# Kernel tuning notes

Measured on AMD Instinct MI355X. Metric: run time of the kernel, lower is better.

The kernel has to match this reference:

```python
import jax, jax.numpy as jnp
import numpy as np

B, C, H, W = 16, 384, 64, 64
S, R, GR = 16, 8, 64
EPS = 1e-6


def setup_inputs() -> dict:
    key = jax.random.key(0)
    ks = jax.random.split(key, 16)
    def rn(k, shape, s):
        return jax.random.normal(k, shape, dtype=jnp.float32) * s
    inp = {"x": jax.random.normal(ks[0], (B, C, H, W), dtype=jnp.float32)}
    i = 1
    for p in ("row", "col"):
        inp[p + "_a_logit"] = jnp.zeros((S,), jnp.float32)
        inp[p + "_U"] = rn(ks[i], (S, R), 0.02); i += 1
        inp[p + "_V"] = rn(ks[i], (S, R), 0.02); i += 1
        inp[p + "_Win"] = rn(ks[i], (S, C), 1.0 / np.sqrt(C)); i += 1
        inp[p + "_bin"] = jnp.zeros((S,), jnp.float32)
        inp[p + "_Wg"] = rn(ks[i], (S, C), 1.0 / np.sqrt(C)); i += 1
        inp[p + "_bg"] = jnp.zeros((S,), jnp.float32)
        inp[p + "_Wout"] = rn(ks[i], (C, S), 1.0 / np.sqrt(S)); i += 1
        inp[p + "_bout"] = jnp.zeros((C,), jnp.float32)
        inp[p + "_Wskip"] = rn(ks[i], (C, C), 1.0 / np.sqrt(C)); i += 1
        inp[p + "_bskip"] = jnp.zeros((C,), jnp.float32)
    inp["g1_w"] = rn(ks[i], (GR, C), 1.0 / np.sqrt(C)); i += 1
    inp["g1_b"] = jnp.zeros((GR,), jnp.float32)
    inp["g2_w"] = rn(ks[i], (C, GR), 1.0 / np.sqrt(GR)); i += 1
    inp["g2_b"] = jnp.zeros((C,), jnp.float32)
    inp["norm_w"] = jnp.ones((C,), jnp.float32)
    inp["norm_b"] = jnpp = jnp.zeros((C,), jnp.float32)
    inp["norm_b"] = jnp.zeros((C,), jnp.float32)
    return inp


def _ssm1d(x, a_logit, U, V, Win, bin_, Wg, bg, Wout, bout, Wskip, bskip, reverse):
    # x: [N, L, D]
    if reverse:
        x = x[:, ::-1]
    u = jnp.einsum('nld,sd->nls', x, Win) + bin_          # [N,L,S]
    g = jax.nn.sigmoid(jnp.einsum('nld,sd->nls', x, Wg) + bg)
    a = jax.nn.sigmoid(a_logit)                            # [S]
    # h_t = a*h + g_t*u_t + h @ (U V^T)^T  ==  h @ (diag(a) + (U V^T)^T) + g_t*u_t
    A = jnp.diag(a) + (U @ V.T).T                          # [S,S]
    gu = jnp.swapaxes(g * u, 0, 1)                         # [L,N,S]
    h0 = jnp.zeros((x.shape[0], a.shape[0]), x.dtype)

    def step(h, gu_t):
        h = h @ A + gu_t
        return h, h

    _, hs = jax.lax.scan(step, h0, gu)                     # [L,N,S]
    hs = jnp.swapaxes(hs, 0, 1)                            # [N,L,S]
    y = (jnp.einsum('nls,ds->nld', hs, Wout) + bout
         + jnp.einsum('nld,ed->nle', x, Wskip) + bskip)
    if reverse:
        y = y[:, ::-1]
    return y


def _forward(x, rp, cp, g1_w, g1_b, g2_w, g2_b, norm_w, norm_b):
    Bx, Cx, Hx, Wx = x.shape
    rows = jnp.transpose(x, (0, 2, 3, 1)).reshape(Bx * Hx, Wx, Cx)
    cols = jnp.transpose(x, (0, 3, 2, 1)).reshape(Bx * Wx, Hx, Cx)
    yr = _ssm1d(rows, *rp, False) + _ssm1d(rows, *rp, True)
    yc = _ssm1d(cols, *cp, False) + _ssm1d(cols, *cp, True)
    yr = jnp.transpose(yr.reshape(Bx, Hx, Wx, Cx), (0, 3, 1, 2))
    yc = jnp.transpose(yc.reshape(Bx, Wx, Hx, Cx), (0, 3, 2, 1))
    y = (yr + yc) * 0.25
    # LayerNorm over channel dim of BCHW
    mean = x.mean(axis=1, keepdims=True)
    var = ((x - mean) ** 2).mean(axis=1, keepdims=True)
    xn = (x - mean) / jnp.sqrt(var + EPS)
    xn = xn * norm_w[None, :, None, None] + norm_b[None, :, None, None]
    # gate: 1x1 conv -> GELU(exact) -> 1x1 conv -> sigmoid
    h1 = jax.nn.gelu(jnp.einsum('bchw,oc->bohw', xn, g1_w) + g1_b[None, :, None, None], approximate=False)
    g = jax.nn.sigmoid(jnp.einsum('bghw,cg->bchw', h1, g2_w) + g2_b[None, :, None, None])
    return g * y + (1.0 - g) * x


def reference(x, row_a_logit, row_U, row_V, row_Win, row_bin, row_Wg, row_bg, row_Wout, row_bout, row_Wskip, row_bskip, col_a_logit, col_U, col_V, col_Win, col_bin, col_Wg, col_bg, col_Wout, col_bout, col_Wskip, col_bskip, g1_w, g1_b, g2_w, g2_b, norm_w, norm_b):
    rp = (row_a_logit, row_U, row_V, row_Win, row_bin, row_Wg, row_bg, row_Wout, row_bout, row_Wskip, row_bskip)
    cp = (col_a_logit, col_U, col_V, col_Win, col_bin, col_Wg, col_bg, col_Wout, col_bout, col_Wskip, col_bskip)
    return _forward(x, rp, cp, g1_w, g1_b, g2_w, g2_b, norm_w, norm_b)
```

## Files before the change

### kernel.cpp

```cpp
#include <hip/hip_runtime.h>
#include <hip/hip_bf16.h>
#include <math.h>

#define PP 4096
#define CCH 384
#define NB 16

using short8 = __attribute__((ext_vector_type(8))) short;
using f32x4  = __attribute__((ext_vector_type(4))) float;
using half2t = __attribute__((ext_vector_type(2))) __fp16;

__device__ __forceinline__ float sigmoidf_(float v){ return 1.f/(1.f+expf(-v)); }
__device__ __forceinline__ float fast_sig(float v){
  return __builtin_amdgcn_rcpf(1.f + __builtin_amdgcn_exp2f(-v*1.44269504088896f));
}
__device__ __forceinline__ unsigned int f2bf(float f){
  __hip_bfloat16 h = __float2bfloat16(f);
  return (unsigned int)*reinterpret_cast<unsigned short*>(&h);
}
__device__ __forceinline__ float bf2f(unsigned short u){
  unsigned int w = ((unsigned int)u) << 16;
  return __uint_as_float(w);
}
__device__ __forceinline__ void gload_lds16(const void* g, void* l){
  __builtin_amdgcn_global_load_lds(
      (const __attribute__((address_space(1))) unsigned int*)g,
      (__attribute__((address_space(3))) unsigned int*)l, 16, 0, 0);
}

__global__ __launch_bounds__(256) void k_prep(
    const float* __restrict__ rAl, const float* __restrict__ rU, const float* __restrict__ rV,
    const float* __restrict__ cAl, const float* __restrict__ cU, const float* __restrict__ cV,
    const float* __restrict__ rWs, const float* __restrict__ cWs,
    const float* __restrict__ WinR, const float* __restrict__ WgR,
    const float* __restrict__ WinC, const float* __restrict__ WgC,
    const float* __restrict__ g1w, const float* __restrict__ nw, const float* __restrict__ nb,
    const float* __restrict__ g2w,
    const float* __restrict__ WoR, const float* __restrict__ WoC,
    float* __restrict__ Arow, float* __restrict__ Acol,
    unsigned short* __restrict__ WsumBf, unsigned short* __restrict__ WcatBf,
    unsigned short* __restrict__ g2wBf, unsigned short* __restrict__ WocatBf,
    float* __restrict__ t1, float* __restrict__ t2)
{
  int bid = blockIdx.x, tid = threadIdx.x;
  if (bid < 576) {
    int idx = bid*256 + tid;
    WsumBf[idx] = (unsigned short)f2bf(rWs[idx] + cWs[idx]);
  } else if (bid < 768) {
    int idx = (bid-576)*256 + tid;
    int row = idx / CCH, col = idx - row*CCH;
    float v;
    if      (row < 16)  v = WinR[row*CCH + col];
    else if (row < 32)  v = WgR [(row-16)*CCH + col];
    else if (row < 48)  v = WinC[(row-32)*CCH + col];
    else if (row < 64)  v = WgC [(row-48)*CCH + col];
    else                v = g1w[(row-64)*CCH + col]*nw[col];
    WcatBf[idx] = (unsigned short)f2bf(v);
  } else if (bid < 864) {
    int idx = (bid-768)*256 + tid;
    g2wBf[idx] = (unsigned short)f2bf(g2w[idx]);
  } else if (bid < 960) {
    int idx = (bid-864)*256 + tid;
    int c = idx >> 6, k = idx & 63;
    int sel = (k >> 4) & 1;
    float v = 0.5f * (sel ? WoC[c*16 + (k&15)] : WoR[c*16 + (k&15)]);
    WocatBf[idx] = (unsigned short)f2bf(v);
  } else {
    {
      int i = tid >> 4, j = tid & 15;
      float sr = 0.f, sc = 0.f;
      #pragma unroll
      for (int r=0;r<8;++r){ sr += rV[i*8+r]*rU[j*8+r]; sc += cV[i*8+r]*cU[j*8+r]; }
      if (i==j){ sr += sigmoidf_(rAl[i]); sc += sigmoidf_(cAl[i]); }
      Arow[tid] = sr; Acol[tid] = sc;
    }
    if (tid < 64) {
      float s1=0.f, s2=0.f;
      for (int c=0;c<CCH;++c){ s1 += g1w[tid*CCH+c]*nw[c]; s2 += nb[c]*g1w[tid*CCH+c]; }
      t1[tid]=s1; t2[tid]=s2;
    }
  }
}

__global__ __launch_bounds__(256) void k_xf(
    const float* __restrict__ x, const unsigned short* __restrict__ WcatBf,
    const float* __restrict__ binR, const float* __restrict__ bgR,
    const float* __restrict__ binC, const float* __restrict__ bgC,
    const float* __restrict__ t1, const float* __restrict__ t2,
    const float* __restrict__ g1b,
    unsigned short* __restrict__ xbf,
    float* __restrict__ ugr, float* __restrict__ ugc,
    unsigned short* __restrict__ h1bf)
{
  int b = blockIdx.x >> 6, pt = blockIdx.x & 63;
  int t = threadIdx.x;
  int w = t >> 6, l = t & 63;
  int lr = l & 15, kq = l >> 4, kb8 = kq*8;
  int pl = t & 63, g4 = w;

  __shared__ unsigned short xtb[2][64*64];
  __shared__ float red[512];
  __shared__ float meanS[64], invS[64];

  const float* xb = x + (size_t)b*CCH*PP + pt*64;
  f32x4 acc[2][4] = {};
  float sx = 0.f, sx2 = 0.f;

  const unsigned short* wrow0 = WcatBf + (size_t)(w*32 + lr)*CCH + kb8;
  const unsigned short* wrow1 = wrow0 + 16*CCH;
  unsigned short* xgo = xbf + ((size_t)(b*PP + pt*64))*CCH;

  float xv[16];
  #pragma unroll
  for (int j=0;j<16;++j) xv[j] = xb[(size_t)(g4*16 + j)*PP + pl];

  {
    unsigned int pk[8];
    #pragma unroll
    for (int j=0;j<16;++j){ sx += xv[j]; sx2 += xv[j]*xv[j]; }
    #pragma unroll
    for (int j=0;j<8;++j) pk[j] = f2bf(xv[2*j]) | (f2bf(xv[2*j+1])<<16);
    int kg0 = g4*2, kg1 = g4*2+1;
    *(uint4*)&xtb[0][(size_t)(pl*8 + (kg0 ^ (pl&7)))*8] = make_uint4(pk[0],pk[1],pk[2],pk[3]);
    *(uint4*)&xtb[0][(size_t)(pl*8 + (kg1 ^ (pl&7)))*8] = make_uint4(pk[4],pk[5],pk[6],pk[7]);
  }
  #pragma unroll
  for (int j=0;j<16;++j) xv[j] = xb[(size_t)(64 + g4*16 + j)*PP + pl];
  __syncthreads();

  #pragma unroll
  for (int cc=0; cc<6; ++cc) {
    int cur = cc & 1;
    if (cc < 5) {
      unsigned int pk[8];
      #pragma unroll
      for (int j=0;j<16;++j){ sx += xv[j]; sx2 += xv[j]*xv[j]; }
      #pragma unroll
      for (int j=0;j<8;++j) pk[j] = f2bf(xv[2*j]) | (f2bf(xv[2*j+1])<<16);
      int kg0 = g4*2, kg1 = g4*2+1;
      *(uint4*)&xtb[cur^1][(size_t)(pl*8 + (kg0 ^ (pl&7)))*8] = make_uint4(pk[0],pk[1],pk[2],pk[3]);
      *(uint4*)&xtb[cur^1][(size_t)(pl*8 + (kg1 ^ (pl&7)))*8] = make_uint4(pk[4],pk[5],pk[6],pk[7]);
      if (cc < 4) {
        #pragma unroll
        for (int j=0;j<16;++j) xv[j] = xb[(size_t)((cc+2)*64 + g4*16 + j)*PP + pl];
      }
    }
    short8 a0k0 = *(const short8*)(wrow0 + cc*64);
    short8 a0k1 = *(const short8*)(wrow0 + cc*64 + 32);
    short8 a1k0 = *(const short8*)(wrow1 + cc*64);
    short8 a1k1 = *(const short8*)(wrow1 + cc*64 + 32);
    #pragma unroll
    for (int ks=0; ks<2; ++ks){
      int kg = ks*4 + kq;
      #pragma unroll
      for (int nf=0; nf<4; ++nf){
        int pr = nf*16 + lr;
        short8 bv = *(const short8*)&xtb[cur][(size_t)(pr*8 + (kg ^ (pr&7)))*8];
        acc[0][nf] = __builtin_amdgcn_mfma_f32_16x16x32_bf16(ks? a0k1:a0k0, bv, acc[0][nf], 0,0,0);
        acc[1][nf] = __builtin_amdgcn_mfma_f32_16x16x32_bf16(ks? a1k1:a1k0, bv, acc[1][nf], 0,0,0);
      }
    }
    #pragma unroll
    for (int it=0; it<2; ++it){
      int p2 = 32*it + (t>>3), kg2 = t & 7;
      uint4 v = *(const uint4*)&xtb[cur][(size_t)(p2*8 + (kg2 ^ (p2&7)))*8];
      *(uint4*)&xgo[(size_t)p2*CCH + cc*64 + kg2*8] = v;
    }
    __syncthreads();
  }

  red[g4*64 + pl] = sx;
  red[256 + g4*64 + pl] = sx2;
  __syncthreads();
  if (t < 64) {
    float s1 = red[t] + red[64+t] + red[128+t] + red[192+t];
    float s2 = red[256+t] + red[320+t] + red[384+t] + red[448+t];
    float mu = s1 * (1.f/CCH);
    float var = s2 * (1.f/CCH) - mu*mu;
    meanS[t] = mu;
    invS[t]  = rsqrtf(var + 1e-6f);
  }
  __syncthreads();

  if (w < 2) {
    const float* bu = w ? binC : binR;
    const float* bg = w ? bgC  : bgR;
    float* dst = w ? ugc : ugr;
    float bus[4], bgs[4];
    #pragma unroll
    for (int r=0;r<4;++r){ int s = kq*4 + r; bus[r]=bu[s]; bgs[r]=bg[s]; }
    #pragma unroll
    for (int nf=0; nf<4; ++nf){
      size_t pbase = ((size_t)(b*PP + pt*64 + nf*16 + lr))*16;
      #pragma unroll
      for (int r=0;r<4;++r){
        int s = kq*4 + r;
        float u = acc[0][nf][r] + bus[r];
        float g = fast_sig(acc[1][nf][r] + bgs[r]);
        dst[pbase + s] = u*g;
      }
    }
  } else {
    int ob = (w-2)*32 + kq*4;
    float t1o[2][4], t2o[2][4], gbo[2][4];
    #pragma unroll
    for (int mi=0;mi<2;++mi)
      #pragma unroll
      for (int r=0;r<4;++r){
        int o = ob + mi*16 + r;
        t1o[mi][r]=t1[o]; t2o[mi][r]=t2[o]; gbo[mi][r]=g1b[o];
      }
    #pragma unroll
    for (int nf=0; nf<4; ++nf){
      int pLoc = nf*16 + lr;
      float mu = meanS[pLoc], iv = invS[pLoc];
      #pragma unroll
      for (int mi=0;mi<2;++mi){
        unsigned int us[4];
        #pragma unroll
        for (int r=0;r<4;++r){
          float pre = iv*(acc[mi][nf][r] - mu*t1o[mi][r]) + t2o[mi][r] + gbo[mi][r];
          float aa = pre*(1.f + 0.044715f*pre*pre);
          float ge = pre*fast_sig(1.5957691216f*aa);
          us[r] = f2bf(ge);
        }
        uint2 o2; o2.x = us[0] | (us[1]<<16); o2.y = us[2] | (us[3]<<16);
        *reinterpret_cast<uint2*>(h1bf + ((size_t)(b*PP + pt*64 + pLoc))*64 + (w-2)*32 + mi*16 + kq*4) = o2;
      }
    }
  }
}

__global__ __launch_bounds__(256) void k_scan(
    const float* __restrict__ ugr, const float* __restrict__ ugc,
    const float* __restrict__ Arow, const float* __restrict__ Acol,
    unsigned short* __restrict__ hs2)
{
  int Wv = blockIdx.x*4 + (threadIdx.x >> 6);
  int lane = threadIdx.x & 63;
  int tsk = Wv*2 + (lane >> 5);
  int base32 = lane & 32;
  int half = (lane >> 4) & 1, s = lane & 15;
  int dir = tsk >> 11;
  int rem = tsk & 2047;
  int isCol = rem >> 10;
  int gg = rem & 1023;
  int b = gg >> 6, rc = gg & 63;
  const float* ug = isCol ? ugc : ugr;
  const float* A  = isCol ? Acol : Arow;
  int off = dir*32 + isCol*16;
  int p0 = b*PP + (isCol ? rc : rc*64);
  int stride = isCol ? 64 : 1;
  float ac[8];
  #pragma unroll
  for (int i=0;i<8;++i) ac[i] = A[(half*8 + i)*16 + s];
  float h = 0.f;
  int l2_0 = dir ? 63 : 0;
  float gu = ug[((size_t)(p0 + l2_0*stride))*16 + s];
  #pragma unroll 4
  for (int st=0; st<64; ++st){
    int l2 = dir ? (63-st) : st;
    float gu_next = 0.f;
    if (st < 63){
      int l2n = dir ? (62-st) : (st+1);
      gu_next = ug[((size_t)(p0 + l2n*stride))*16 + s];
    }
    float part = 0.f;
    #pragma unroll
    for (int i=0;i<8;++i) part += __shfl(h, base32 + half*8 + i, 64) * ac[i];
    float tt = part + __shfl_xor(part, 16, 64);
    h = tt + gu;
    if (!(lane & 16))
      hs2[((size_t)(p0 + l2*stride))*64 + off + s] = (unsigned short)f2bf(h);
    gu = gu_next;
  }
}

__global__ __launch_bounds__(512, 4) void k_fused(
    const unsigned short* __restrict__ xbf,
    const unsigned short* __restrict__ WsumBf,
    const unsigned short* __restrict__ h1bf, const unsigned short* __restrict__ g2wBf,
    const unsigned short* __restrict__ hs2, const unsigned short* __restrict__ WocatBf,
    const float* __restrict__ g2b,
    const float* __restrict__ boR, const float* __restrict__ bsR,
    const float* __restrict__ boC, const float* __restrict__ bsC,
    float* __restrict__ outp)
{
  int obid = blockIdx.x;
  int bid = ((obid & 7) * 128) + (obid >> 3);
  int b = bid >> 6, pt = bid & 63;
  int t = threadIdx.x;
  int w = t >> 6, l = t & 63;
  int lr = l & 15, kq = l >> 4, kb8 = kq * 8;
  int cw = w*48;

  __shared__ unsigned short xt[64*48*8];

  short8 gaw[3][2], gbv[2][4];
  {
    const unsigned short* hbase = h1bf + ((size_t)(b*PP + pt*64 + lr))*64 + kb8;
    #pragma unroll
    for (int ks=0; ks<2; ++ks)
      #pragma unroll
      for (int nf=0; nf<4; ++nf)
        gbv[ks][nf] = *(const short8*)(hbase + (size_t)nf*16*64 + ks*32);
    #pragma unroll
    for (int mi=0; mi<3; ++mi){
      const unsigned short* wbg = g2wBf + (size_t)(cw + mi*16 + lr)*64 + kb8;
      gaw[mi][0] = *(const short8*)(wbg);
      gaw[mi][1] = *(const short8*)(wbg + 32);
    }
  }
  short8 hv[2][4];
  {
    const unsigned short* hb2 = hs2 + ((size_t)(b*PP + pt*64 + lr))*64 + kb8;
    #pragma unroll
    for (int ks=0;ks<2;++ks)
      #pragma unroll
      for (int nf=0;nf<4;++nf)
        hv[ks][nf] = *(const short8*)(hb2 + (size_t)nf*16*64 + ks*32);
  }

  {
    const unsigned short* xrow0 = xbf + ((size_t)(b*PP + pt*64))*CCH;
    #pragma unroll
    for (int i=0;i<6;++i){
      int G = w*384 + i*64 + l;
      int p = G/48, kgs = G - p*48;
      int kg = (kgs & ~7) | ((kgs & 7) ^ (p & 7));
      gload_lds16(xrow0 + (size_t)p*CCH + kg*8, &xt[(size_t)G*8]);
    }
  }

  unsigned int gt[3][4][2];
  {
    f32x4 gac[3][4] = {};
    #pragma unroll
    for (int ks=0; ks<2; ++ks)
      #pragma unroll
      for (int nf=0; nf<4; ++nf)
        #pragma unroll
        for (int mi=0; mi<3; ++mi)
          gac[mi][nf] = __builtin_amdgcn_mfma_f32_16x16x32_bf16(gaw[mi][ks], gbv[ks][nf], gac[mi][nf], 0,0,0);
    #pragma unroll
    for (int mi=0;mi<3;++mi){
      float4 gb4 = *(const float4*)&g2b[cw + mi*16 + kq*4];
      #pragma unroll
      for (int nf=0;nf<4;++nf){
        float s0 = fast_sig(gac[mi][nf][0] + gb4.x);
        float s1 = fast_sig(gac[mi][nf][1] + gb4.y);
        float s2 = fast_sig(gac[mi][nf][2] + gb4.z);
        float s3 = fast_sig(gac[mi][nf][3] + gb4.w);
        half2t p01 = __builtin_amdgcn_cvt_pkrtz(s0, s1);
        half2t p23 = __builtin_amdgcn_cvt_pkrtz(s2, s3);
        __builtin_memcpy(&gt[mi][nf][0], &p01, 4);
        __builtin_memcpy(&gt[mi][nf][1], &p23, 4);
      }
    }
  }

  __syncthreads();

  f32x4 acc[3][4] = {};
  const unsigned short* wbS = WsumBf + (size_t)(cw + lr)*CCH + kb8;
  #pragma unroll
  for (int c=0;c<6;++c){
    short8 a[3][2];
    #pragma unroll
    for (int mi=0;mi<3;++mi){
      a[mi][0] = *(const short8*)(wbS + (size_t)mi*16*CCH + c*64);
      a[mi][1] = *(const short8*)(wbS + (size_t)mi*16*CCH + c*64 + 32);
    }
    #pragma unroll
    for (int ks=0;ks<2;++ks){
      int kgl = ks*4 + kq;
      #pragma unroll
      for (int nf=0;nf<4;++nf){
        int pr = nf*16 + lr;
        int kgs = c*8 + (kgl ^ (pr & 7));
        short8 bv = *(const short8*)&xt[(size_t)(pr*48 + kgs)*8];
        #pragma unroll
        for (int mi=0;mi<3;++mi)
          acc[mi][nf] = __builtin_amdgcn_mfma_f32_16x16x32_bf16(a[mi][ks], bv, acc[mi][nf], 0,0,0);
      }
    }
  }

  {
    #pragma unroll
    for (int mi=0;mi<3;++mi){
      const unsigned short* wo = WocatBf + (size_t)(cw + mi*16 + lr)*64 + kb8;
      short8 wa0 = *(const short8*)(wo);
      short8 wa1 = *(const short8*)(wo + 32);
      #pragma unroll
      for (int nf=0;nf<4;++nf){
        acc[mi][nf] = __builtin_amdgcn_mfma_f32_16x16x32_bf16(wa0, hv[0][nf], acc[mi][nf], 0,0,0);
        acc[mi][nf] = __builtin_amdgcn_mfma_f32_16x16x32_bf16(wa1, hv[1][nf], acc[mi][nf], 0,0,0);
      }
    }
  }

  #pragma unroll
  for (int mi=0;mi<3;++mi){
    int cb0 = cw + mi*16 + kq*4;
    float4 b1 = *(const float4*)&boR[cb0];
    float4 b2 = *(const float4*)&bsR[cb0];
    float4 b3 = *(const float4*)&boC[cb0];
    float4 b4 = *(const float4*)&bsC[cb0];
    float cb4[4] = { b1.x+b2.x+b3.x+b4.x, b1.y+b2.y+b3.y+b4.y,
                     b1.z+b2.z+b3.z+b4.z, b1.w+b2.w+b3.w+b4.w };
    int kgR = cb0 >> 3, eoff = cb0 & 7;
    #pragma unroll
    for (int nf=0;nf<4;++nf){
      int p = nf*16 + lr;
      int kgsR = (kgR & ~7) | ((kgR & 7) ^ (p & 7));
      uint2 xres = *(const uint2*)&xt[(size_t)(p*48 + kgsR)*8 + eoff];
      half2t g01, g23;
      __builtin_memcpy(&g01, &gt[mi][nf][0], 4);
      __builtin_memcpy(&g23, &gt[mi][nf][1], 4);
      float gv[4] = { (float)g01[0], (float)g01[1], (float)g23[0], (float)g23[1] };
      #pragma unroll
      for (int r=0;r<4;++r){
        unsigned int word = (r < 2) ? xres.x : xres.y;
        unsigned short us = (r & 1) ? (unsigned short)(word >> 16) : (unsigned short)(word & 0xffff);
        float xv = bf2f(us);
        float y = 0.5f*acc[mi][nf][r] + 0.5f*cb4[r];
        float gtv = gv[r];
        size_t addr = ((size_t)(b*CCH + cb0 + r))*PP + pt*64 + p;
        outp[addr] = gtv*y + (1.f-gtv)*xv;
      }
    }
  }
}

extern "C" void kernel_launch(void* const* d_in, const int* in_sizes, int n_in,
                              void* d_out, int out_size, void* d_ws, size_t ws_size,
                              hipStream_t stream)
{
  const float* x    = (const float*)d_in[0];
  const float* rAl  = (const float*)d_in[1];
  const float* rU   = (const float*)d_in[2];
  const float* rV   = (const float*)d_in[3];
  const float* rWin = (const float*)d_in[4];
  const float* rbin = (const float*)d_in[5];
  const float* rWg  = (const float*)d_in[6];
  const float* rbg  = (const float*)d_in[7];
  const float* rWo  = (const float*)d_in[8];
  const float* rbo  = (const float*)d_in[9];
  const float* rWs  = (const float*)d_in[10];
  const float* rbs  = (const float*)d_in[11];
  const float* cAl  = (const float*)d_in[12];
  const float* cU   = (const float*)d_in[13];
  const float* cV   = (const float*)d_in[14];
  const float* cWin = (const float*)d_in[15];
  const float* cbin = (const float*)d_in[16];
  const float* cWg  = (const float*)d_in[17];
  const float* cbg  = (const float*)d_in[18];
  const float* cWo  = (const float*)d_in[19];
  const float* cbo  = (const float*)d_in[20];
  const float* cWs  = (const float*)d_in[21];
  const float* cbs  = (const float*)d_in[22];
  const float* g1w  = (const float*)d_in[23];
  const float* g1b  = (const float*)d_in[24];
  const float* g2w  = (const float*)d_in[25];
  const float* g2b  = (const float*)d_in[26];
  const float* nw   = (const float*)d_in[27];
  const float* nb   = (const float*)d_in[28];

  float* ws   = (float*)d_ws;
  float* ugr  = ws;
  float* ugc  = ugr + 1048576;
  float* Arow = ugc + 1048576;
  float* Acol = Arow + 256;
  float* t1   = Acol + 256;
  float* t2   = t1 + 64;
  unsigned short* xbf     = (unsigned short*)(t2 + 64);
  unsigned short* h1bf    = xbf + (size_t)25165824;
  unsigned short* hs2     = h1bf + (size_t)4194304;
  unsigned short* WsumBf  = hs2 + (size_t)4194304;
  unsigned short* WcatBf  = WsumBf + 147456;
  unsigned short* g2wBf   = WcatBf + 49152;
  unsigned short* WocatBf = g2wBf + 24576;
  float* outp = (float*)d_out;

  k_prep<<<961, 256, 0, stream>>>(rAl,rU,rV,cAl,cU,cV,rWs,cWs,
                                  rWin,rWg,cWin,cWg,g1w,nw,nb,g2w,rWo,cWo,
                                  Arow,Acol,WsumBf,WcatBf,g2wBf,WocatBf,t1,t2);
  k_xf<<<1024, 256, 0, stream>>>(x, WcatBf, rbin, rbg, cbin, cbg,
                                 t1, t2, g1b, xbf, ugr, ugc, h1bf);
  k_scan<<<512, 256, 0, stream>>>(ugr, ugc, Arow, Acol, hs2);
  k_fused<<<1024, 512, 0, stream>>>(xbf, WsumBf, h1bf, g2wBf,
                                    hs2, WocatBf, g2b,
                                    rbo, rbs, cbo, cbs, outp);
}
```

Measured before the change: 172.0 us.

## Halve LDS tile by staging x in two K-halves to raise occupancy

```diff
diff --git a/kernel.cpp b/kernel.cpp
--- a/kernel.cpp
+++ b/kernel.cpp
@@ -276,7 +276,7 @@
   }
 }
 
-__global__ __launch_bounds__(512, 4) void k_fused(
+__global__ __launch_bounds__(512, 8) void k_fused(
     const unsigned short* __restrict__ xbf,
     const unsigned short* __restrict__ WsumBf,
     const unsigned short* __restrict__ h1bf, const unsigned short* __restrict__ g2wBf,
@@ -294,7 +294,9 @@
   int lr = l & 15, kq = l >> 4, kb8 = kq * 8;
   int cw = w*48;
 
-  __shared__ unsigned short xt[64*48*8];
+  __shared__ unsigned short xt[64*24*8];
+
+  const unsigned short* xrow0 = xbf + ((size_t)(b*PP + pt*64))*CCH;
 
   short8 gaw[3][2], gbv[2][4];
   {
@@ -311,25 +313,13 @@
       gaw[mi][1] = *(const short8*)(wbg + 32);
     }
   }
-  short8 hv[2][4];
-  {
-    const unsigned short* hb2 = hs2 + ((size_t)(b*PP + pt*64 + lr))*64 + kb8;
-    #pragma unroll
-    for (int ks=0;ks<2;++ks)
-      #pragma unroll
-      for (int nf=0;nf<4;++nf)
-        hv[ks][nf] = *(const short8*)(hb2 + (size_t)nf*16*64 + ks*32);
-  }
-
-  {
-    const unsigned short* xrow0 = xbf + ((size_t)(b*PP + pt*64))*CCH;
-    #pragma unroll
-    for (int i=0;i<6;++i){
-      int G = w*384 + i*64 + l;
-      int p = G/48, kgs = G - p*48;
-      int kg = (kgs & ~7) | ((kgs & 7) ^ (p & 7));
-      gload_lds16(xrow0 + (size_t)p*CCH + kg*8, &xt[(size_t)G*8]);
-    }
+
+  #pragma unroll
+  for (int i=0;i<3;++i){
+    int G = w*192 + i*64 + l;
+    int p = G/24, kgs = G - p*24;
+    int kg = (kgs & ~7) | ((kgs & 7) ^ (p & 7));
+    gload_lds16(xrow0 + (size_t)p*CCH + kg*8, &xt[(size_t)G*8]);
   }
 
   unsigned int gt[3][4][2];
@@ -363,8 +353,11 @@
 
   f32x4 acc[3][4] = {};
   const unsigned short* wbS = WsumBf + (size_t)(cw + lr)*CCH + kb8;
-  #pragma unroll
-  for (int c=0;c<6;++c){
+  uint2 xres[4];
+  int cb0q = cw + kq*4;
+
+  #pragma unroll
+  for (int c=0;c<3;++c){
     short8 a[3][2];
     #pragma unroll
     for (int mi=0;mi<3;++mi){
@@ -378,15 +371,85 @@
       for (int nf=0;nf<4;++nf){
         int pr = nf*16 + lr;
         int kgs = c*8 + (kgl ^ (pr & 7));
-        short8 bv = *(const short8*)&xt[(size_t)(pr*48 + kgs)*8];
+        short8 bv = *(const short8*)&xt[(size_t)(pr*24 + kgs)*8];
         #pragma unroll
         for (int mi=0;mi<3;++mi)
           acc[mi][nf] = __builtin_amdgcn_mfma_f32_16x16x32_bf16(a[mi][ks], bv, acc[mi][nf], 0,0,0);
       }
     }
   }
+  uint2 xresAll[3][4];
+  if (w < 4) {
+    #pragma unroll
+    for (int mi=0;mi<3;++mi){
+      int cb0 = cb0q + mi*16;
+      int kgR = cb0 >> 3, eoff = cb0 & 7;
+      #pragma unroll
+      for (int nf=0;nf<4;++nf){
+        int p = nf*16 + lr;
+        int kgsR = (kgR & ~7) | ((kgR & 7) ^ (p & 7));
+        xresAll[mi][nf] = *(const uint2*)&xt[(size_t)(p*24 + kgsR)*8 + eoff];
+      }
+    }
+  }
+  (void)xres;
+
+  __syncthreads();
+
+  #pragma unroll
+  for (int i=0;i<3;++i){
+    int G = w*192 + i*64 + l;
+    int p = G/24, kgs = G - p*24;
+    int kg = (kgs & ~7) | ((kgs & 7) ^ (p & 7));
+    gload_lds16(xrow0 + (size_t)p*CCH + 192 + kg*8, &xt[(size_t)G*8]);
+  }
+
+  __syncthreads();
+
+  #pragma unroll
+  for (int c=0;c<3;++c){
+    short8 a[3][2];
+    #pragma unroll
+    for (int mi=0;mi<3;++mi){
+      a[mi][0] = *(const short8*)(wbS + (size_t)mi*16*CCH + (c+3)*64);
+      a[mi][1] = *(const short8*)(wbS + (size_t)mi*16*CCH + (c+3)*64 + 32);
+    }
+    #pragma unroll
+    for (int ks=0;ks<2;++ks){
+      int kgl = ks*4 + kq;
+      #pragma unroll
+      for (int nf=0;nf<4;++nf){
+        int pr = nf*16 + lr;
+        int kgs = c*8 + (kgl ^ (pr & 7));
+        short8 bv = *(const short8*)&xt[(size_t)(pr*24 + kgs)*8];
+        #pragma unroll
+        for (int mi=0;mi<3;++mi)
+          acc[mi][nf] = __builtin_amdgcn_mfma_f32_16x16x32_bf16(a[mi][ks], bv, acc[mi][nf], 0,0,0);
+      }
+    }
+  }
+  if (w >= 4) {
+    #pragma unroll
+    for (int mi=0;mi<3;++mi){
+      int cb0 = cb0q + mi*16 - 192;
+      int kgR = cb0 >> 3, eoff = cb0 & 7;
+      #pragma unroll
+      for (int nf=0;nf<4;++nf){
+        int p = nf*16 + lr;
+        int kgsR = (kgR & ~7) | ((kgR & 7) ^ (p & 7));
+        xresAll[mi][nf] = *(const uint2*)&xt[(size_t)(p*24 + kgsR)*8 + eoff];
+      }
+    }
+  }
 
   {
+    const unsigned short* hb2 = hs2 + ((size_t)(b*PP + pt*64 + lr))*64 + kb8;
+    short8 hv[2][4];
+    #pragma unroll
+    for (int ks=0;ks<2;++ks)
+      #pragma unroll
+      for (int nf=0;nf<4;++nf)
+        hv[ks][nf] = *(const short8*)(hb2 + (size_t)nf*16*64 + ks*32);
     #pragma unroll
     for (int mi=0;mi<3;++mi){
       const unsigned short* wo = WocatBf + (size_t)(cw + mi*16 + lr)*64 + kb8;
@@ -409,19 +472,17 @@
     float4 b4 = *(const float4*)&bsC[cb0];
     float cb4[4] = { b1.x+b2.x+b3.x+b4.x, b1.y+b2.y+b3.y+b4.y,
                      b1.z+b2.z+b3.z+b4.z, b1.w+b2.w+b3.w+b4.w };
-    int kgR = cb0 >> 3, eoff = cb0 & 7;
     #pragma unroll
     for (int nf=0;nf<4;++nf){
       int p = nf*16 + lr;
-      int kgsR = (kgR & ~7) | ((kgR & 7) ^ (p & 7));
-      uint2 xres = *(const uint2*)&xt[(size_t)(p*48 + kgsR)*8 + eoff];
+      uint2 xr = xresAll[mi][nf];
       half2t g01, g23;
       __builtin_memcpy(&g01, &gt[mi][nf][0], 4);
       __builtin_memcpy(&g23, &gt[mi][nf][1], 4);
       float gv[4] = { (float)g01[0], (float)g01[1], (float)g23[0], (float)g23[1] };
       #pragma unroll
       for (int r=0;r<4;++r){
-        unsigned int word = (r < 2) ? xres.x : xres.y;
+        unsigned int word = (r < 2) ? xr.x : xr.y;
         unsigned short us = (r & 1) ? (unsigned short)(word >> 16) : (unsigned short)(word & 0xffff);
         float xv = bf2f(us);
         float y = 0.5f*acc[mi][nf][r] + 0.5f*cb4[r];
```

New measurement: 543.1 us. 216% more time.
